# Performance work log

Hardware: AMD Instinct MI355X
Metric: run time of the kernel (lower is better)

The kernel has to match this reference:

```python
import jax, jax.numpy as jnp
import numpy as np

B, P, S, CTX = 64, 10, 200, 512
H, NH, DH = 512, 4, 128      # hidden_dim, num_heads, head_dim
ROLE, NUMR = 32, 10
OUT = 2
T = 100                      # max_steps
LSTM_IN = OUT + 2 + ROLE + CTX  # 548


def setup_inputs() -> dict:
    key = jax.random.key(0)
    ks = jax.random.split(key, 32)
    std = 0.02
    f = jnp.float32
    inp = {
        'context_sequence': jax.random.normal(ks[0], (B, P, S, CTX), f),
        'initial_position': jax.random.normal(ks[1], (B, P, OUT), f),
        'ball_landing': jax.random.normal(ks[2], (B, OUT), f),
        'roles': jax.random.randint(ks[3], (B, P), 0, NUMR),
        'max_steps': T,
        # params
        'role_emb': jax.random.normal(ks[4], (NUMR, ROLE), f) * std,
        'Wc': jax.random.normal(ks[5], (H, CTX), f) * std,
        'bc': jnp.zeros((H,), f),
        'Wq': jax.random.normal(ks[6], (H, H), f) * std,
        'bq': jnp.zeros((H,), f),
        'Wk': jax.random.normal(ks[7], (H, H), f) * std,
        'bk': jnp.zeros((H,), f),
        'Wv': jax.random.normal(ks[8], (H, H), f) * std,
        'bv': jnp.zeros((H,), f),
        'Wo': jax.random.normal(ks[9], (H, H), f) * std,
        'bo': jnp.zeros((H,), f),
        'W_ih0': jax.random.normal(ks[10], (4 * H, LSTM_IN), f) * std,
        'W_hh0': jax.random.normal(ks[11], (4 * H, H), f) * std,
        'b_ih0': jnp.zeros((4 * H,), f),
        'b_hh0': jnp.zeros((4 * H,), f),
        'W_ih1': jax.random.normal(ks[12], (4 * H, H), f) * std,
        'W_hh1': jax.random.normal(ks[13], (4 * H, H), f) * std,
        'b_ih1': jnp.zeros((4 * H,), f),
        'b_hh1': jnp.zeros((4 * H,), f),
        'Wf1': jax.random.normal(ks[14], (H // 2, H), f) * std,
        'bf1': jnp.zeros((H // 2,), f),
        'Wf2': jax.random.normal(ks[15], (OUT, H // 2), f) * std,
        'bf2': jnp.zeros((OUT,), f),
    }
    return inp


def _lstm_cell(x, h, c, Wih, Whh, bih, bhh):
    # torch gate order: i, f, g, o
    g = x @ Wih.T + bih + h @ Whh.T + bhh
    i, fg, gg, o = jnp.split(g, 4, axis=-1)
    cn = jax.nn.sigmoid(fg) * c + jax.nn.sigmoid(i) * jnp.tanh(gg)
    hn = jax.nn.sigmoid(o) * jnp.tanh(cn)
    return hn, cn


def reference(context_sequence, initial_position, ball_landing, roles, max_steps,
              role_emb, Wc, bc, Wq, bq, Wk, bk, Wv, bv, Wo, bo,
              W_ih0, W_hh0, b_ih0, b_hh0, W_ih1, W_hh1, b_ih1, b_hh1,
              Wf1, bf1, Wf2, bf2):
    b, p, s, ctx = context_sequence.shape
    n = b * p
    dt = context_sequence.dtype
    scale = 1.0 / np.sqrt(DH)

    # project context once; hoist K,V (keys/values are constant across steps)
    ctx_proj = context_sequence.reshape(n, s, ctx) @ Wc.T + bc          # [N,S,H]
    K = (ctx_proj @ Wk.T + bk).reshape(n, s, NH, DH)                    # [N,S,h,d]
    V = (ctx_proj @ Wv.T + bv).reshape(n, s, NH, DH)

    role_e = role_emb[roles.reshape(-1)]                                # [N,ROLE]
    ball = jnp.broadcast_to(ball_landing[:, None, :], (b, p, OUT)).reshape(n, OUT)
    pos0 = initial_position.reshape(n, OUT)
    h0 = jnp.zeros((2, n, H), dt)
    c0 = jnp.zeros((2, n, H), dt)

    def step(carry, _):
        h, c, pos = carry
        # query: current pos zero-padded to context_dim, then context_proj
        qin = jnp.concatenate([pos, jnp.zeros((n, ctx - OUT), dt)], axis=-1)
        qp = qin @ Wc.T + bc                                            # [N,H]
        q = (qp @ Wq.T + bq).reshape(n, NH, DH)
        scores = jnp.einsum('nhd,nshd->nhs', q, K) * scale
        w = jax.nn.softmax(scores, axis=-1)
        att = jnp.einsum('nhs,nshd->nhd', w, V).reshape(n, H)
        att = att @ Wo.T + bo                                           # [N,H]
        x = jnp.concatenate([pos, ball, role_e, att], axis=-1)          # [N,548]
        h0n, c0n = _lstm_cell(x, h[0], c[0], W_ih0, W_hh0, b_ih0, b_hh0)
        h1n, c1n = _lstm_cell(h0n, h[1], c[1], W_ih1, W_hh1, b_ih1, b_hh1)
        hid = jax.nn.relu(h1n @ Wf1.T + bf1)
        nxt = hid @ Wf2.T + bf2                                         # [N,2]
        return (jnp.stack([h0n, h1n]), jnp.stack([c0n, c1n]), nxt), nxt

    _, preds = jax.lax.scan(step, (h0, c0, pos0), None, length=max_steps)
    # [T,N,2] -> [B,P,T,2]
    return preds.transpose(1, 0, 2).reshape(b, p, max_steps, OUT)
```

## Files before the change

### kernel.cpp

```cpp
#include <hip/hip_runtime.h>
#include <hip/hip_bf16.h>
#include <cstddef>


typedef _Float16 hx8 __attribute__((ext_vector_type(8)));
typedef float fx4 __attribute__((ext_vector_type(4)));
typedef unsigned long long u64;

#define NSEQ 640
#define TSTEPS 100
#define XC0 1088
#define XC1 1024
#define NBLK 640
#define FL 32

__device__ __forceinline__ float sigm(float x){ return 1.0f/(1.0f+__expf(-x)); }
__device__ __forceinline__ float tanh_(float x){
  x = fminf(fmaxf(x, -15.0f), 15.0f);
  float e = __expf(2.0f*x);
  return (e-1.0f)/(e+1.0f);
}
__device__ __forceinline__ float sel4(float a0,float a1,float a2,float a3,int h){
  float r = a0; r = (h==1)?a1:r; r = (h==2)?a2:r; r = (h==3)?a3:r; return r;
}

__device__ __forceinline__ hx8 ldA(const _Float16* p){
  u64 q0 = __hip_atomic_load((u64*)p,     __ATOMIC_RELAXED, __HIP_MEMORY_SCOPE_AGENT);
  u64 q1 = __hip_atomic_load((u64*)p + 1, __ATOMIC_RELAXED, __HIP_MEMORY_SCOPE_AGENT);
  union { u64 q[2]; hx8 v; } u; u.q[0]=q0; u.q[1]=q1;
  return u.v;
}


__global__ void kF1(const float* __restrict__ Wq, const float* __restrict__ Wc,
                    const float* __restrict__ bc, const float* __restrict__ bq,
                    float* __restrict__ u){
  int r = blockIdx.x*256 + threadIdx.x; if (r >= 512) return;
  float s0=0.f, s1=0.f, s2=0.f;
  for (int k=0;k<512;k++){
    float wq = Wq[r*512+k];
    s0 += wq*Wc[k*512+0];
    s1 += wq*Wc[k*512+1];
    s2 += wq*bc[k];
  }
  u[r]=s0; u[512+r]=s1; u[1024+r]=s2+bq[r];
}

__global__ __launch_bounds__(512) void kF2a(const float* __restrict__ Wk,
                                            const float* __restrict__ u,
                                            float* __restrict__ z){
  int ih = blockIdx.x; int kk = threadIdx.x;
  int i = ih>>2, h = ih&3;
  float s = 0.f;
  for (int d=0; d<128; d++)
    s += Wk[(h*128+d)*512 + kk] * u[i*512 + h*128 + d];
  z[ih*512+kk] = s;
}

__global__ __launch_bounds__(512) void kF2b(const float* __restrict__ z,
                                            const float* __restrict__ Wc,
                                            const float* __restrict__ bc,
                                            const float* __restrict__ bk,
                                            const float* __restrict__ u,
                                            float* __restrict__ Y, float* __restrict__ cc){
  const float scale = 0.08838834764831845f;
  int ih = blockIdx.x; int j = threadIdx.x;
  int i = ih>>2, h = ih&3;
  float s = 0.f;
  for (int kk=0;kk<512;kk++) s += z[ih*512+kk]*Wc[kk*512+j];
  Y[ih*512+j] = s*scale;
  if (j==0){
    float t=0.f;
    for (int kk=0;kk<512;kk++) t += z[ih*512+kk]*bc[kk];
    for (int d=0;d<128;d++) t += u[i*512+h*128+d]*bk[h*128+d];
    cc[ih] = t*scale;
  }
}

__global__ void kFbv(const float* __restrict__ Wv, const float* __restrict__ bc,
                     const float* __restrict__ bv, float* __restrict__ bv2){
  int r = blockIdx.x*256 + threadIdx.x; if (r >= 512) return;
  float s = bv[r];
  for (int k=0;k<512;k++) s += Wv[r*512+k]*bc[k];
  bv2[r]=s;
}

__global__ __launch_bounds__(256) void kgemm(const float* __restrict__ A, int lda, int aoff,
                                             const float* __restrict__ B, int ldb,
                                             float* __restrict__ C, int ldc, int K){
  __shared__ float As[64][16];
  __shared__ float Bs[16][64];
  int tid = threadIdx.x; int tx = tid&15, ty = tid>>4;
  int bx = blockIdx.x, by = blockIdx.y;
  float acc[4][4];
#pragma unroll
  for (int i=0;i<4;i++)
#pragma unroll
    for (int j=0;j<4;j++) acc[i][j]=0.f;
  for (int kk=0; kk<K; kk+=16){
#pragma unroll
    for (int e=0;e<4;e++){
      int id = tid*4+e;
      int r = id>>4, c = id&15;
      As[r][c] = A[(size_t)(by*64+r)*lda + aoff + kk + c];
      int r2 = id>>6, c2 = id&63;
      Bs[r2][c2] = B[(size_t)(kk+r2)*ldb + bx*64 + c2];
    }
    __syncthreads();
#pragma unroll
    for (int k=0;k<16;k++){
      float bvv[4];
#pragma unroll
      for (int j=0;j<4;j++) bvv[j] = Bs[k][tx*4+j];
#pragma unroll
      for (int i=0;i<4;i++){
        float av = As[ty*4+i][k];
#pragma unroll
        for (int j=0;j<4;j++) acc[i][j] += av*bvv[j];
      }
    }
    __syncthreads();
  }
#pragma unroll
  for (int i=0;i<4;i++)
#pragma unroll
    for (int j=0;j<4;j++)
      C[(size_t)(by*64+ty*4+i)*ldc + bx*64+tx*4+j] = acc[i][j];
}

__global__ void ktransp(const float* __restrict__ A, float* __restrict__ AT){
  int idx = blockIdx.x*256 + threadIdx.x;
  int r = idx>>9, c = idx&511;
  AT[c*512 + r] = A[idx];
}

__global__ void kbcat0(const float* __restrict__ Wih0, const float* __restrict__ Wmix,
                       const float* __restrict__ Whh0, _Float16* __restrict__ B){
  int r = blockIdx.x;
  for (int c = threadIdx.x; c < 1088; c += 256){
    float v;
    if (c < 36) v = Wih0[r*548 + c];
    else if (c < 548) v = Wmix[r*512 + (c-36)];
    else if (c < 576) v = 0.f;
    else v = Whh0[r*512 + (c-576)];
    B[(size_t)r*1088 + c] = (_Float16)v;
  }
}

__global__ void kbcat1(const float* __restrict__ Wih1, const float* __restrict__ Whh1,
                       _Float16* __restrict__ B){
  int r = blockIdx.x;
  for (int c = threadIdx.x; c < 1024; c += 256){
    float v = (c < 512) ? Wih1[r*512 + c] : Whh1[r*512 + (c-512)];
    B[(size_t)r*1024 + c] = (_Float16)v;
  }
}

__global__ void kcast(const float* __restrict__ s, _Float16* __restrict__ d, int n){
  int i = blockIdx.x*256 + threadIdx.x;
  if (i < n) d[i] = (_Float16)s[i];
}

__global__ void kbias(const float* __restrict__ Wih0, const float* __restrict__ bo,
                      const float* __restrict__ bih0, const float* __restrict__ bhh0,
                      const float* __restrict__ bih1, const float* __restrict__ bhh1,
                      float* __restrict__ b0, float* __restrict__ b1){
  int j = blockIdx.x*256 + threadIdx.x; if (j >= 2048) return;
  float s = bih0[j]+bhh0[j];
  for (int k=0;k<512;k++) s += Wih0[j*548+36+k]*bo[k];
  b0[j]=s; b1[j]=bih1[j]+bhh1[j];
}


__global__ __launch_bounds__(256) void kP1(const float* __restrict__ ctx,
                                           const float* __restrict__ Y,
                                           const float* __restrict__ cc,
                                           float* __restrict__ W6){
  __shared__ float Yl[6144];
  __shared__ float ccl[12];
  int tid = threadIdx.x; int n = blockIdx.x;
  for (int e = tid; e < 6144; e += 256) Yl[e] = Y[e];
  if (tid < 12) ccl[tid] = cc[tid];
  __syncthreads();
  int wave = tid >> 6, lane = tid & 63;
  for (int it = 0; it < 50; ++it){
    int s = it*4 + wave;
    const float* cp = ctx + ((size_t)n*200 + s)*512;
    float p[12];
#pragma unroll
    for (int i=0;i<12;i++) p[i]=0.f;
    for (int c8 = 0; c8 < 8; ++c8){
      int col = c8*64 + lane;
      float v = cp[col];
#pragma unroll
      for (int i=0;i<12;i++) p[i] += v * Yl[i*512+col];
    }
#pragma unroll
    for (int m = 32; m; m >>= 1){
#pragma unroll
      for (int i=0;i<12;i++) p[i] += __shfl_xor(p[i], m, 64);
    }
    if (lane < 4){
      int h = lane;
      float a  = sel4(p[0],p[1],p[2], p[3], h) + ccl[h];
      float b  = sel4(p[4],p[5],p[6], p[7], h) + ccl[4+h];
      float cp_= sel4(p[8],p[9],p[10],p[11],h) + ccl[8+h];
      float beta = __expf(cp_);
      size_t base = (size_t)(n*24 + h*6)*200 + s;
      W6[base + 0*200] = beta;
      W6[base + 1*200] = beta*a;
      W6[base + 2*200] = beta*b;
      W6[base + 3*200] = beta*a*a*0.5f;
      W6[base + 4*200] = beta*a*b;
      W6[base + 5*200] = beta*b*b*0.5f;
    }
  }
}

__global__ __launch_bounds__(256) void kP2(const float* __restrict__ ctx,
                                           const float* __restrict__ W6,
                                           float* __restrict__ F, float* __restrict__ S){
  __shared__ float w6[4800];
  int tid = threadIdx.x, n = blockIdx.x;
  for (int e = tid; e < 4800; e += 256) w6[e] = W6[(size_t)n*4800 + e];
  __syncthreads();
  float a0[24], a1[24];
#pragma unroll
  for (int r=0;r<24;r++){ a0[r]=0.f; a1[r]=0.f; }
  const float* cp = ctx + (size_t)n*200*512;
  for (int s=0;s<200;s++){
    float v0 = cp[s*512 + tid];
    float v1 = cp[s*512 + tid + 256];
#pragma unroll
    for (int r=0;r<24;r++){ float w = w6[r*200+s]; a0[r]+=w*v0; a1[r]+=w*v1; }
  }
#pragma unroll
  for (int r=0;r<24;r++){
    F[(size_t)(n*24+r)*512 + tid]       = a0[r];
    F[(size_t)(n*24+r)*512 + tid + 256] = a1[r];
  }
  if (tid < 24){
    float s=0.f;
    for (int ss=0; ss<200; ss++) s += w6[tid*200+ss];
    S[n*24+tid]=s;
  }
}

__global__ __launch_bounds__(128) void kP3(const float* __restrict__ F,
                                           const float* __restrict__ WcvT,
                                           float* __restrict__ M){
  __shared__ float Fl[3072];
  int tid = threadIdx.x; int b = blockIdx.x; int n = b>>2, h = b&3;
  for (int e = tid; e < 3072; e += 128) Fl[e] = F[(size_t)(n*24 + h*6)*512 + e];
  __syncthreads();
  float acc[6];
#pragma unroll
  for (int i=0;i<6;i++) acc[i]=0.f;
  for (int k=0;k<512;k++){
    float w = WcvT[k*512 + h*128 + tid];
#pragma unroll
    for (int i=0;i<6;i++) acc[i] += w * Fl[i*512+k];
  }
#pragma unroll
  for (int i=0;i<6;i++) M[(size_t)(n*24+h*6+i)*128 + tid] = acc[i];
}


__global__ __launch_bounds__(512) void kinit(const float* __restrict__ ball,
                    const int* __restrict__ roles, const float* __restrict__ remb,
                    _Float16* __restrict__ x0, _Float16* __restrict__ x1,
                    _Float16* __restrict__ hc0, _Float16* __restrict__ hc1,
                    float* __restrict__ c0, float* __restrict__ c1,
                    unsigned* __restrict__ bar){
  int n = blockIdx.x, tid = threadIdx.x;
  int b = n/10;
  int role = roles[n];
  for (int c = tid; c < XC0; c += 512){
    float v = 0.f;
    if (c>=2 && c<4)       v = ball[b*2 + (c-2)];
    else if (c>=4 && c<36) v = remb[role*32 + (c-4)];
    _Float16 hv = (_Float16)v;
    x0[(size_t)n*XC0+c] = hv;
    x1[(size_t)n*XC0+c] = hv;
  }
  for (int c = tid; c < XC1; c += 512){
    hc0[(size_t)n*XC1+c] = (_Float16)0.f;
    hc1[(size_t)n*XC1+c] = (_Float16)0.f;
  }
  for (int e = tid; e < 512; e += 512){
    c0[n*512+e]=0.f; c1[n*512+e]=0.f;
  }
  if (tid < FL) bar[n*FL + tid] = 0u;
}

__global__ __launch_bounds__(128) void katt0(const float* __restrict__ ipos,
                                             const float* __restrict__ M,
                                             const float* __restrict__ S,
                                             const float* __restrict__ bv2,
                                             _Float16* __restrict__ x){
  int n = blockIdx.x, tid = threadIdx.x;
  float p0 = ipos[n*2], p1 = ipos[n*2+1];
  if (tid==0){ x[(size_t)n*XC0]=(_Float16)p0; x[(size_t)n*XC0+1]=(_Float16)p1; }
  float fa=p0*p0, fb=p0*p1, fc=p1*p1;
  for (int hd = tid; hd < 512; hd += 128){
    int h = hd>>7;
    int sb = n*24 + h*6;
    float den = S[sb] + p0*S[sb+1] + p1*S[sb+2] + fa*S[sb+3] + fb*S[sb+4] + fc*S[sb+5];
    const float* mp = M + (size_t)sb*128 + (hd&127);
    float num = mp[0] + p0*mp[128] + p1*mp[256] + fa*mp[384] + fb*mp[512] + fc*mp[640];
    x[(size_t)n*XC0 + 36 + hd] = (_Float16)(num/den + bv2[hd]);
  }
}


template<int NC>
__device__ __forceinline__ void gates_body(
    const _Float16* __restrict__ A, int lda,
    const _Float16* __restrict__ B,
    const float* __restrict__ bias, float* __restrict__ cst,
    _Float16* __restrict__ h1p, int ldh1, int co1,
    _Float16* __restrict__ h2p, int ldh2, int co2,
    int bx, _Float16* sbase, float (*eps)[32][16]){
  int tid = threadIdx.x, w = tid>>6, lane = tid&63;
  int lr = lane&15, lq = lane>>4;
  int mblk = bx>>5, jb = bx&31;
  int m0 = mblk*32, j0 = jb*16;
  int li = lane>>3, lc = lane&7;
  const _Float16* gA  = A + (size_t)(m0 + w*8 + li)*lda + lc*8;
  const _Float16* gB0 = B + (size_t)(w*512 + j0 + li)*lda + lc*8;
  const _Float16* gB1 = B + (size_t)(w*512 + j0 + 8 + li)*lda + lc*8;
  int sA  = (w*8 + li)*64        + ((lc ^ li)<<3);
  int sB0 = 2048 + (w*16 + li)*64 + ((lc ^ li)<<3);
  int sB1 = 2048 + (w*16 + 8 + li)*64 + ((lc ^ li)<<3);
  int ra7 = lr & 7;
  int fA00 = lr*64        + (((lq  ) ^ ra7)<<3);
  int fA01 = lr*64        + (((lq+4) ^ ra7)<<3);
  int fA10 = (16+lr)*64   + (((lq  ) ^ ra7)<<3);
  int fA11 = (16+lr)*64   + (((lq+4) ^ ra7)<<3);
  int fB0  = 2048 + (w*16+lr)*64 + (((lq  ) ^ ra7)<<3);
  int fB1  = 2048 + (w*16+lr)*64 + (((lq+4) ^ ra7)<<3);
  hx8 pA[3], pB0[3], pB1[3];
#pragma unroll
  for (int i=0;i<3;i++){
    int k = i*64;
    pA[i]  = ldA(gA + k);
    pB0[i] = *(const hx8*)(gB0 + k);
    pB1[i] = *(const hx8*)(gB1 + k);
  }
  fx4 ac0={0.f,0.f,0.f,0.f}, ac1={0.f,0.f,0.f,0.f};
#pragma unroll
  for (int c=0; c<NC; ++c){
    const int s = c % 3;
    _Float16* sb = sbase + (c&1)*6144;
    *(hx8*)(sb + sA)  = pA[s];
    *(hx8*)(sb + sB0) = pB0[s];
    *(hx8*)(sb + sB1) = pB1[s];
    __syncthreads();
    if (c+3 < NC){
      int k = (c+3)*64;
      pA[s]  = ldA(gA + k);
      pB0[s] = *(const hx8*)(gB0 + k);
      pB1[s] = *(const hx8*)(gB1 + k);
    }
    hx8 b0 = *(const hx8*)(sb + fB0);
    hx8 a0 = *(const hx8*)(sb + fA00);
    hx8 a1 = *(const hx8*)(sb + fA10);
    ac0 = __builtin_amdgcn_mfma_f32_16x16x32_f16(a0, b0, ac0, 0,0,0);
    ac1 = __builtin_amdgcn_mfma_f32_16x16x32_f16(a1, b0, ac1, 0,0,0);
    hx8 b1  = *(const hx8*)(sb + fB1);
    hx8 a0b = *(const hx8*)(sb + fA01);
    hx8 a1b = *(const hx8*)(sb + fA11);
    ac0 = __builtin_amdgcn_mfma_f32_16x16x32_f16(a0b, b1, ac0, 0,0,0);
    ac1 = __builtin_amdgcn_mfma_f32_16x16x32_f16(a1b, b1, ac1, 0,0,0);
  }
#pragma unroll
  for (int r=0;r<4;r++){
    eps[w][lq*4+r][lr]    = ac0[r];
    eps[w][16+lq*4+r][lr] = ac1[r];
  }
  __syncthreads();
#pragma unroll
  for (int e=0;e<2;e++){
    int idx = e*256 + tid;
    int ml = idx>>4, j = idx&15;
    float gi = eps[0][ml][j] + bias[       j0+j];
    float gf = eps[1][ml][j] + bias[ 512 + j0+j];
    float gg = eps[2][ml][j] + bias[1024 + j0+j];
    float go = eps[3][ml][j] + bias[1536 + j0+j];
    int ci = (m0+ml)*512 + j0 + j;
    float c_ = cst[ci];
    float cn = sigm(gf)*c_ + sigm(gi)*tanh_(gg);
    float hn = sigm(go)*tanh_(cn);
    cst[ci] = cn;
    _Float16 hh = (_Float16)hn;
    h1p[(size_t)(m0+ml)*ldh1 + co1 + j0 + j] = hh;
    if (h2p) h2p[(size_t)(m0+ml)*ldh2 + co2 + j0 + j] = hh;
  }
}

template<int NC>
__global__ __launch_bounds__(256) void kgates(
    const _Float16* A, int lda, const _Float16* B,
    const float* bias, float* cst,
    _Float16* h1p, int ldh1, int co1,
    _Float16* h2p, int ldh2, int co2){
  __shared__ __align__(16) char smem[32768];
  gates_body<NC>(A, lda, B, bias, cst, h1p, ldh1, co1, h2p, ldh2, co2,
                 blockIdx.x, (_Float16*)smem, (float(*)[32][16])(smem + 24576));
}

__device__ __forceinline__ void s3_body(const _Float16* __restrict__ h1, int ldh,
    const _Float16* __restrict__ Wf1, const float* __restrict__ bf1,
    const float* __restrict__ Wf2, const float* __restrict__ bf2,
    const float* __restrict__ M, const float* __restrict__ S,
    const float* __restrict__ bv2, _Float16* __restrict__ xn,
    float* __restrict__ out, int t, int n0,
    float (*hid)[264], float (*posL)[2], float (*denL)[4]){
  int tid = threadIdx.x, w = tid>>6, lane = tid&63;
  int lr = lane&15, lq = lane>>4;
  fx4 acc[4];
#pragma unroll
  for (int c=0;c<4;c++) acc[c] = (fx4){0.f,0.f,0.f,0.f};
  {
    const _Float16* ap = h1 + (size_t)(n0+lr)*ldh + lq*8;
    for (int ks=0; ks<16; ks++){
      hx8 a = ldA(ap + ks*32);
#pragma unroll
      for (int c=0;c<4;c++){
        const _Float16* bp = Wf1 + (size_t)(w*64 + c*16 + lr)*512 + ks*32 + lq*8;
        acc[c] = __builtin_amdgcn_mfma_f32_16x16x32_f16(a, *(const hx8*)bp, acc[c], 0,0,0);
      }
    }
  }
#pragma unroll
  for (int c=0;c<4;c++)
#pragma unroll
    for (int r=0;r<4;r++){
      int col = w*64 + c*16 + lr;
      hid[lq*4+r][col] = fmaxf(acc[c][r] + bf1[col], 0.f);
    }
  __syncthreads();
  {
    int nn = tid>>4, o = (tid>>3)&1, sub = tid&7;
    float s = 0.f;
#pragma unroll
    for (int k2=0;k2<32;k2++) s += hid[nn][k2*8 + sub] * Wf2[o*256 + k2*8 + sub];
    s += __shfl_xor(s, 1, 64);
    s += __shfl_xor(s, 2, 64);
    s += __shfl_xor(s, 4, 64);
    if (sub==0){
      s += bf2[o];
      out[((size_t)(n0+nn)*TSTEPS + t)*2 + o] = s;
      posL[nn][o] = s;
      xn[(size_t)(n0+nn)*XC0 + o] = (_Float16)s;
    }
  }
  __syncthreads();
  if (tid < 64){
    int nn = tid>>2, h = tid&3;
    float p0 = posL[nn][0], p1 = posL[nn][1];
    int sb = (n0+nn)*24 + h*6;
    float den = S[sb] + p0*S[sb+1] + p1*S[sb+2] + p0*p0*S[sb+3] + p0*p1*S[sb+4] + p1*p1*S[sb+5];
    denL[nn][h] = 1.0f/den;
  }
  __syncthreads();
#pragma unroll
  for (int half=0; half<2; half++){
    int hd = half*256 + tid;
    int h = hd>>7, d = hd&127;
    for (int nn=0; nn<16; nn++){
      float p0 = posL[nn][0], p1 = posL[nn][1];
      float fa = p0*p0, fb = p0*p1, fc = p1*p1;
      const float* mp = M + (size_t)((n0+nn)*24 + h*6)*128 + d;
      float num = mp[0] + p0*mp[128] + p1*mp[256] + fa*mp[384] + fb*mp[512] + fc*mp[640];
      xn[(size_t)(n0+nn)*XC0 + 36 + hd] = (_Float16)(num*denL[nn][h] + bv2[hd]);
    }
  }
}

__global__ __launch_bounds__(256) void ks3b(const _Float16* __restrict__ h1, int ldh,
    const _Float16* __restrict__ Wf1, const float* __restrict__ bf1,
    const float* __restrict__ Wf2, const float* __restrict__ bf2,
    const float* __restrict__ M, const float* __restrict__ S,
    const float* __restrict__ bv2, _Float16* __restrict__ xn,
    float* __restrict__ out, int t){
  __shared__ float hid[16][264];
  __shared__ float posL[16][2];
  __shared__ float denL[16][4];
  s3_body(h1, ldh, Wf1, bf1, Wf2, bf2, M, S, bv2, xn, out, t,
          blockIdx.x*16, hid, posL, denL);
}


__device__ __forceinline__ void garrive(unsigned* bar, int bx, unsigned val){
  __syncthreads();
  if (threadIdx.x == 0)
    __hip_atomic_store(bar + (size_t)bx*FL, val, __ATOMIC_RELEASE,
                       __HIP_MEMORY_SCOPE_AGENT);
}
__device__ __forceinline__ void gwait(unsigned* bar, int bx, unsigned val){
  if (threadIdx.x < 64){
    const unsigned* fp = bar + (size_t)((bx & ~31) + (threadIdx.x & 31))*FL;
    for(;;){
      unsigned v = __hip_atomic_load((unsigned*)fp, __ATOMIC_RELAXED,
                                     __HIP_MEMORY_SCOPE_AGENT);
      if (__ballot(v >= val) == ~0ull) break;
      __builtin_amdgcn_s_sleep(2);
    }
  }
  __syncthreads();
}
__device__ __forceinline__ void gbar32(unsigned* bar, int bx, unsigned val){
  garrive(bar, bx, val);
  gwait(bar, bx, val);
}

struct LoopArgs {
  const _Float16* B0; const _Float16* B1;
  const float* b0; const float* b1;
  float* c0; float* c1;
  _Float16* x0; _Float16* x1; _Float16* h0; _Float16* h1;
  const _Float16* Wf1; const float* bf1; const float* Wf2; const float* bf2;
  const float* M; const float* S; const float* bv2;
  float* out; unsigned* bar;
};

__global__ __launch_bounds__(256, 3) void kloop(LoopArgs a){
  __shared__ __align__(16) char smem[32768];
  _Float16* sbase = (_Float16*)smem;
  float (*eps)[32][16] = (float(*)[32][16])(smem + 24576);
  float (*hid)[264] = (float(*)[264])smem;
  float (*posL)[2] = (float(*)[2])(smem + 16896);
  float (*denL)[4] = (float(*)[4])(smem + 17024);
  int bid = blockIdx.x;
  int mblk = bid>>5, jb = bid&31;
  for (int t = 0; t < TSTEPS; ++t){
    unsigned bb = (unsigned)(t*3);
    _Float16* xin = (t&1) ? a.x1 : a.x0;
    _Float16* xnx = (t&1) ? a.x0 : a.x1;
    _Float16* hin = (t&1) ? a.h1 : a.h0;
    _Float16* hnx = (t&1) ? a.h0 : a.h1;
    gates_body<17>(xin, XC0, a.B0, a.b0, a.c0, hin, XC1, 0, xnx, XC0, 576,
                   bid, sbase, eps);
    gbar32(a.bar, bid, bb+1);
    gates_body<16>(hin, XC1, a.B1, a.b1, a.c1, hnx, XC1, 512,
                   (_Float16*)0, 0, 0, bid, sbase, eps);
    if (jb < 2){
      gbar32(a.bar, bid, bb+2);
      s3_body(hnx + 512, XC1, a.Wf1, a.bf1, a.Wf2, a.bf2, a.M, a.S, a.bv2,
              xnx, a.out, t, mblk*32 + jb*16, hid, posL, denL);
    }
    gbar32(a.bar, bid, bb+3);
  }
}


extern "C" void kernel_launch(void* const* d_in, const int* in_sizes, int n_in,
                              void* d_out, int out_size, void* d_ws, size_t ws_size,
                              hipStream_t stream) {
  const float* ctx   = (const float*)d_in[0];
  const float* ipos  = (const float*)d_in[1];
  const float* ball  = (const float*)d_in[2];
  const int*   roles = (const int*)  d_in[3];
  const float* remb  = (const float*)d_in[5];
  const float* Wc    = (const float*)d_in[6];
  const float* bc    = (const float*)d_in[7];
  const float* Wq    = (const float*)d_in[8];
  const float* bq    = (const float*)d_in[9];
  const float* Wk    = (const float*)d_in[10];
  const float* bk    = (const float*)d_in[11];
  const float* Wv    = (const float*)d_in[12];
  const float* bv    = (const float*)d_in[13];
  const float* Wo    = (const float*)d_in[14];
  const float* bo    = (const float*)d_in[15];
  const float* Wih0  = (const float*)d_in[16];
  const float* Whh0  = (const float*)d_in[17];
  const float* bih0  = (const float*)d_in[18];
  const float* bhh0  = (const float*)d_in[19];
  const float* Wih1  = (const float*)d_in[20];
  const float* Whh1  = (const float*)d_in[21];
  const float* bih1  = (const float*)d_in[22];
  const float* bhh1  = (const float*)d_in[23];
  const float* Wf1   = (const float*)d_in[24];
  const float* bf1   = (const float*)d_in[25];
  const float* Wf2   = (const float*)d_in[26];
  const float* bf2   = (const float*)d_in[27];
  float* out = (float*)d_out;

  char* w = (char*)d_ws;
  auto alloc = [&](size_t bytes){ void* p = (void*)w; w += (bytes + 255) & ~(size_t)255; return p; };
  float* fY    = (float*)alloc(12*512*4);
  float* fcc   = (float*)alloc(12*4);
  float* fu    = (float*)alloc(3*512*4);
  float* fz    = (float*)alloc(12*512*4);
  float* fbv2  = (float*)alloc(512*4);
  float* fWcv  = (float*)alloc((size_t)512*512*4);
  float* fWcvT = (float*)alloc((size_t)512*512*4);
  float* fWmix = (float*)alloc((size_t)2048*512*4);
  _Float16* hB0  = (_Float16*)alloc((size_t)2048*XC0*2);
  _Float16* hB1  = (_Float16*)alloc((size_t)2048*XC1*2);
  _Float16* hWf1 = (_Float16*)alloc((size_t)256*512*2);
  float* fb0 = (float*)alloc(2048*4);
  float* fb1 = (float*)alloc(2048*4);
  float* fW6 = (float*)alloc((size_t)NSEQ*24*200*4);
  float* fS  = (float*)alloc((size_t)NSEQ*24*4);
  float* fF  = (float*)alloc((size_t)NSEQ*24*512*4);
  float* fM  = (float*)alloc((size_t)NSEQ*24*128*4);
  _Float16* xc0 = (_Float16*)alloc((size_t)NSEQ*XC0*2);
  _Float16* xc1 = (_Float16*)alloc((size_t)NSEQ*XC0*2);
  _Float16* hc0 = (_Float16*)alloc((size_t)NSEQ*XC1*2);
  _Float16* hc1 = (_Float16*)alloc((size_t)NSEQ*XC1*2);
  float* fc0 = (float*)alloc((size_t)NSEQ*512*4);
  float* fc1 = (float*)alloc((size_t)NSEQ*512*4);
  unsigned* bar = (unsigned*)alloc((size_t)(NBLK+1)*FL*4);

  kF1 <<<2,  256, 0, stream>>>(Wq, Wc, bc, bq, fu);
  kF2a<<<12, 512, 0, stream>>>(Wk, fu, fz);
  kF2b<<<12, 512, 0, stream>>>(fz, Wc, bc, bk, fu, fY, fcc);
  kFbv<<<2,  256, 0, stream>>>(Wv, bc, bv, fbv2);
  kgemm<<<dim3(8,8),  256, 0, stream>>>(Wv,   512, 0,  Wc, 512, fWcv,  512, 512);
  ktransp<<<1024, 256, 0, stream>>>(fWcv, fWcvT);
  kgemm<<<dim3(8,32), 256, 0, stream>>>(Wih0, 548, 36, Wo, 512, fWmix, 512, 512);
  kbcat0<<<2048, 256, 0, stream>>>(Wih0, fWmix, Whh0, hB0);
  kbcat1<<<2048, 256, 0, stream>>>(Wih1, Whh1, hB1);
  kcast<<<512,  256, 0, stream>>>(Wf1, hWf1, 256*512);
  kbias<<<8, 256, 0, stream>>>(Wih0, bo, bih0, bhh0, bih1, bhh1, fb0, fb1);

  kP1<<<NSEQ, 256, 0, stream>>>(ctx, fY, fcc, fW6);
  kP2<<<NSEQ, 256, 0, stream>>>(ctx, fW6, fF, fS);
  kP3<<<NSEQ*4, 128, 0, stream>>>(fF, fWcvT, fM);

  kinit<<<NSEQ, 512, 0, stream>>>(ball, roles, remb, xc0, xc1, hc0, hc1, fc0, fc1, bar);
  katt0<<<NSEQ, 128, 0, stream>>>(ipos, fM, fS, fbv2, xc0);

  int maxb = 0;
  hipError_t qe = hipOccupancyMaxActiveBlocksPerMultiprocessor(
      &maxb, reinterpret_cast<const void*>(kloop), 256, 0);
  if (qe == hipSuccess && maxb >= 3){
    LoopArgs la;
    la.B0 = hB0; la.B1 = hB1; la.b0 = fb0; la.b1 = fb1;
    la.c0 = fc0; la.c1 = fc1;
    la.x0 = xc0; la.x1 = xc1; la.h0 = hc0; la.h1 = hc1;
    la.Wf1 = hWf1; la.bf1 = bf1; la.Wf2 = Wf2; la.bf2 = bf2;
    la.M = fM; la.S = fS; la.bv2 = fbv2; la.out = out; la.bar = bar;
    kloop<<<NBLK, 256, 0, stream>>>(la);
  } else {
    for (int t = 0; t < TSTEPS; ++t){
      _Float16* xin  = (t&1) ? xc1 : xc0;
      _Float16* xnx  = (t&1) ? xc0 : xc1;
      _Float16* hin  = (t&1) ? hc1 : hc0;
      _Float16* hnx  = (t&1) ? hc0 : hc1;
      kgates<17><<<640, 256, 0, stream>>>(xin, XC0, hB0, fb0, fc0,
                                          hin, XC1, 0, xnx, XC0, 576);
      kgates<16><<<640, 256, 0, stream>>>(hin, XC1, hB1, fb1, fc1,
                                          hnx, XC1, 512, (_Float16*)nullptr, 0, 0);
      ks3b<<<40, 256, 0, stream>>>(hnx + 512, XC1, hWf1, bf1, Wf2, bf2,
                                   fM, fS, fbv2, xnx, out, t);
    }
  }
}
```

Before: 5.110 ms.

## Replace global barriers with fine-grained dataflow flags and split layer-0 K loop

The persistent loop's three barriers per step are replaced with per-block release flags: layer-1 waits only on its 32-block group's layer-0 flags, and the s3 step signals its own flags instead of holding a full barrier. The layer-0 GEMM is split so the h0 recurrent chunks (K chunks 9-16) are computed before waiting on the previous step's s3 output, overlapping that work with the wait. Atomic relaxed loads for A tiles are replaced with plain vector loads, and an acquire fence is added after each wait. Correctness now depends on the flag protocol and on cache visibility of plain loads after the acquire.

```diff
diff --git a/kernel.cpp b/kernel.cpp
--- a/kernel.cpp
+++ b/kernel.cpp
@@ -5,7 +5,6 @@
 
 typedef _Float16 hx8 __attribute__((ext_vector_type(8)));
 typedef float fx4 __attribute__((ext_vector_type(4)));
-typedef unsigned long long u64;
 
 #define NSEQ 640
 #define TSTEPS 100
@@ -22,13 +21,6 @@
 }
 __device__ __forceinline__ float sel4(float a0,float a1,float a2,float a3,int h){
   float r = a0; r = (h==1)?a1:r; r = (h==2)?a2:r; r = (h==3)?a3:r; return r;
-}
-
-__device__ __forceinline__ hx8 ldA(const _Float16* p){
-  u64 q0 = __hip_atomic_load((u64*)p,     __ATOMIC_RELAXED, __HIP_MEMORY_SCOPE_AGENT);
-  u64 q1 = __hip_atomic_load((u64*)p + 1, __ATOMIC_RELAXED, __HIP_MEMORY_SCOPE_AGENT);
-  union { u64 q[2]; hx8 v; } u; u.q[0]=q0; u.q[1]=q1;
-  return u.v;
 }
 
 
@@ -287,10 +279,14 @@
     hc0[(size_t)n*XC1+c] = (_Float16)0.f;
     hc1[(size_t)n*XC1+c] = (_Float16)0.f;
   }
-  for (int e = tid; e < 512; e += 512){
-    c0[n*512+e]=0.f; c1[n*512+e]=0.f;
-  }
-  if (tid < FL) bar[n*FL + tid] = 0u;
+  if (tid < 512){
+    c0[n*512+tid]=0.f; c1[n*512+tid]=0.f;
+  }
+  if (tid < FL){
+    bar[(size_t)n*FL + tid] = 0u;
+    bar[(size_t)(640+n)*FL + tid] = 0u;
+    if (n < 40) bar[(size_t)(1280+n)*FL + tid] = 0u;
+  }
 }
 
 __global__ __launch_bounds__(128) void katt0(const float* __restrict__ ipos,
@@ -313,23 +309,20 @@
 }
 
 
-template<int NC>
-__device__ __forceinline__ void gates_body(
+template<int NCH>
+__device__ __forceinline__ void gates_core(
     const _Float16* __restrict__ A, int lda,
-    const _Float16* __restrict__ B,
-    const float* __restrict__ bias, float* __restrict__ cst,
-    _Float16* __restrict__ h1p, int ldh1, int co1,
-    _Float16* __restrict__ h2p, int ldh2, int co2,
-    int bx, _Float16* sbase, float (*eps)[32][16]){
+    const _Float16* __restrict__ B, int ldb,
+    const int (&ord)[NCH], int m0, int j0,
+    _Float16* __restrict__ sbase, fx4& ac0, fx4& ac1)
+{
   int tid = threadIdx.x, w = tid>>6, lane = tid&63;
   int lr = lane&15, lq = lane>>4;
-  int mblk = bx>>5, jb = bx&31;
-  int m0 = mblk*32, j0 = jb*16;
   int li = lane>>3, lc = lane&7;
   const _Float16* gA  = A + (size_t)(m0 + w*8 + li)*lda + lc*8;
-  const _Float16* gB0 = B + (size_t)(w*512 + j0 + li)*lda + lc*8;
-  const _Float16* gB1 = B + (size_t)(w*512 + j0 + 8 + li)*lda + lc*8;
-  int sA  = (w*8 + li)*64        + ((lc ^ li)<<3);
+  const _Float16* gB0 = B + (size_t)(w*512 + j0 + li)*ldb + lc*8;
+  const _Float16* gB1 = B + (size_t)(w*512 + j0 + 8 + li)*ldb + lc*8;
+  int sA  = (w*8 + li)*64         + ((lc ^ li)<<3);
   int sB0 = 2048 + (w*16 + li)*64 + ((lc ^ li)<<3);
   int sB1 = 2048 + (w*16 + 8 + li)*64 + ((lc ^ li)<<3);
   int ra7 = lr & 7;
@@ -342,23 +335,24 @@
   hx8 pA[3], pB0[3], pB1[3];
 #pragma unroll
   for (int i=0;i<3;i++){
-    int k = i*64;
-    pA[i]  = ldA(gA + k);
-    pB0[i] = *(const hx8*)(gB0 + k);
-    pB1[i] = *(const hx8*)(gB1 + k);
-  }
-  fx4 ac0={0.f,0.f,0.f,0.f}, ac1={0.f,0.f,0.f,0.f};
-#pragma unroll
-  for (int c=0; c<NC; ++c){
+    if (i < NCH){
+      int k = ord[i]*64;
+      pA[i]  = *(const hx8*)(gA  + k);
+      pB0[i] = *(const hx8*)(gB0 + k);
+      pB1[i] = *(const hx8*)(gB1 + k);
+    }
+  }
+#pragma unroll
+  for (int c=0; c<NCH; ++c){
     const int s = c % 3;
     _Float16* sb = sbase + (c&1)*6144;
     *(hx8*)(sb + sA)  = pA[s];
     *(hx8*)(sb + sB0) = pB0[s];
     *(hx8*)(sb + sB1) = pB1[s];
     __syncthreads();
-    if (c+3 < NC){
-      int k = (c+3)*64;
-      pA[s]  = ldA(gA + k);
+    if (c+3 < NCH){
+      int k = ord[c+3]*64;
+      pA[s]  = *(const hx8*)(gA  + k);
       pB0[s] = *(const hx8*)(gB0 + k);
       pB1[s] = *(const hx8*)(gB1 + k);
     }
@@ -373,6 +367,16 @@
     ac0 = __builtin_amdgcn_mfma_f32_16x16x32_f16(a0b, b1, ac0, 0,0,0);
     ac1 = __builtin_amdgcn_mfma_f32_16x16x32_f16(a1b, b1, ac1, 0,0,0);
   }
+}
+
+__device__ __forceinline__ void gates_epi(
+    float (*eps)[32][16], fx4& ac0, fx4& ac1, int m0, int j0,
+    const float* __restrict__ bias, float* __restrict__ cst,
+    _Float16* __restrict__ h1p, int ldh1, int co1,
+    _Float16* __restrict__ h2p, int ldh2, int co2)
+{
+  int tid = threadIdx.x, w = tid>>6, lane = tid&63;
+  int lr = lane&15, lq = lane>>4;
 #pragma unroll
   for (int r=0;r<4;r++){
     eps[w][lq*4+r][lr]    = ac0[r];
@@ -398,17 +402,6 @@
   }
 }
 
-template<int NC>
-__global__ __launch_bounds__(256) void kgates(
-    const _Float16* A, int lda, const _Float16* B,
-    const float* bias, float* cst,
-    _Float16* h1p, int ldh1, int co1,
-    _Float16* h2p, int ldh2, int co2){
-  __shared__ __align__(16) char smem[32768];
-  gates_body<NC>(A, lda, B, bias, cst, h1p, ldh1, co1, h2p, ldh2, co2,
-                 blockIdx.x, (_Float16*)smem, (float(*)[32][16])(smem + 24576));
-}
-
 __device__ __forceinline__ void s3_body(const _Float16* __restrict__ h1, int ldh,
     const _Float16* __restrict__ Wf1, const float* __restrict__ bf1,
     const float* __restrict__ Wf2, const float* __restrict__ bf2,
@@ -424,7 +417,7 @@
   {
     const _Float16* ap = h1 + (size_t)(n0+lr)*ldh + lq*8;
     for (int ks=0; ks<16; ks++){
-      hx8 a = ldA(ap + ks*32);
+      hx8 a = *(const hx8*)(ap + ks*32);
 #pragma unroll
       for (int c=0;c<4;c++){
         const _Float16* bp = Wf1 + (size_t)(w*64 + c*16 + lr)*512 + ks*32 + lq*8;
@@ -476,6 +469,31 @@
       xn[(size_t)(n0+nn)*XC0 + 36 + hd] = (_Float16)(num*denL[nn][h] + bv2[hd]);
     }
   }
+}
+
+
+__global__ __launch_bounds__(256) void kgL0(const _Float16* __restrict__ x,
+    const _Float16* __restrict__ B0, const float* __restrict__ b0,
+    float* __restrict__ c0, _Float16* __restrict__ hin, _Float16* __restrict__ xnx){
+  __shared__ __align__(16) char smem[32768];
+  constexpr int ORD17[17] = {0,1,2,3,4,5,6,7,8,9,10,11,12,13,14,15,16};
+  int bid = blockIdx.x, m0 = (bid>>5)*32, j0 = (bid&31)*16;
+  fx4 ac0={0.f,0.f,0.f,0.f}, ac1={0.f,0.f,0.f,0.f};
+  gates_core<17>(x, XC0, B0, XC0, ORD17, m0, j0, (_Float16*)smem, ac0, ac1);
+  gates_epi((float(*)[32][16])(smem+24576), ac0, ac1, m0, j0, b0, c0,
+            hin, XC1, 0, xnx, XC0, 576);
+}
+
+__global__ __launch_bounds__(256) void kgL1(const _Float16* __restrict__ h,
+    const _Float16* __restrict__ B1, const float* __restrict__ b1,
+    float* __restrict__ c1, _Float16* __restrict__ hnx){
+  __shared__ __align__(16) char smem[32768];
+  constexpr int ORD16[16] = {0,1,2,3,4,5,6,7,8,9,10,11,12,13,14,15};
+  int bid = blockIdx.x, m0 = (bid>>5)*32, j0 = (bid&31)*16;
+  fx4 ac0={0.f,0.f,0.f,0.f}, ac1={0.f,0.f,0.f,0.f};
+  gates_core<16>(h, XC1, B1, XC1, ORD16, m0, j0, (_Float16*)smem, ac0, ac1);
+  gates_epi((float(*)[32][16])(smem+24576), ac0, ac1, m0, j0, b1, c1,
+            hnx, XC1, 512, (_Float16*)nullptr, 0, 0);
 }
 
 __global__ __launch_bounds__(256) void ks3b(const _Float16* __restrict__ h1, int ldh,
@@ -492,27 +510,41 @@
 }
 
 
-__device__ __forceinline__ void garrive(unsigned* bar, int bx, unsigned val){
+__device__ __forceinline__ void arrive_rel(unsigned* flag, unsigned val){
   __syncthreads();
   if (threadIdx.x == 0)
-    __hip_atomic_store(bar + (size_t)bx*FL, val, __ATOMIC_RELEASE,
-                       __HIP_MEMORY_SCOPE_AGENT);
-}
-__device__ __forceinline__ void gwait(unsigned* bar, int bx, unsigned val){
+    __hip_atomic_store(flag, val, __ATOMIC_RELEASE, __HIP_MEMORY_SCOPE_AGENT);
+}
+
+__device__ __forceinline__ void acq_fence(const unsigned* p){
+  unsigned d = __hip_atomic_load(p, __ATOMIC_ACQUIRE, __HIP_MEMORY_SCOPE_AGENT);
+  asm volatile("" :: "v"(d));
+}
+
+__device__ __forceinline__ void wait_group(unsigned* base, unsigned val){
   if (threadIdx.x < 64){
-    const unsigned* fp = bar + (size_t)((bx & ~31) + (threadIdx.x & 31))*FL;
+    const unsigned* p = base + (size_t)(threadIdx.x & 31)*FL;
     for(;;){
-      unsigned v = __hip_atomic_load((unsigned*)fp, __ATOMIC_RELAXED,
-                                     __HIP_MEMORY_SCOPE_AGENT);
+      unsigned v = __hip_atomic_load(p, __ATOMIC_RELAXED, __HIP_MEMORY_SCOPE_AGENT);
       if (__ballot(v >= val) == ~0ull) break;
-      __builtin_amdgcn_s_sleep(2);
-    }
-  }
-  __syncthreads();
-}
-__device__ __forceinline__ void gbar32(unsigned* bar, int bx, unsigned val){
-  garrive(bar, bx, val);
-  gwait(bar, bx, val);
+      __builtin_amdgcn_s_sleep(1);
+    }
+    if (threadIdx.x == 0) acq_fence(base);
+  }
+  __syncthreads();
+}
+
+__device__ __forceinline__ void wait_s3(unsigned* s3f, int m, unsigned val){
+  if (threadIdx.x < 64){
+    const unsigned* p = s3f + (size_t)(2*m + (threadIdx.x & 1))*FL;
+    for(;;){
+      unsigned v = __hip_atomic_load(p, __ATOMIC_RELAXED, __HIP_MEMORY_SCOPE_AGENT);
+      if (__ballot(v >= val) == ~0ull) break;
+      __builtin_amdgcn_s_sleep(1);
+    }
+    if (threadIdx.x == 0) acq_fence(p);
+  }
+  __syncthreads();
 }
 
 struct LoopArgs {
@@ -532,25 +564,40 @@
   float (*hid)[264] = (float(*)[264])smem;
   float (*posL)[2] = (float(*)[2])(smem + 16896);
   float (*denL)[4] = (float(*)[4])(smem + 17024);
+  constexpr int ORD_H0[8] = {9,10,11,12,13,14,15,16};
+  constexpr int ORD_X[9]  = {0,1,2,3,4,5,6,7,8};
+  constexpr int ORD16[16] = {0,1,2,3,4,5,6,7,8,9,10,11,12,13,14,15};
   int bid = blockIdx.x;
-  int mblk = bid>>5, jb = bid&31;
+  int m = bid>>5, jb = bid&31;
+  int m0 = m*32, j0 = jb*16;
+  unsigned* L0own = a.bar + (size_t)bid*FL;
+  unsigned* L1own = a.bar + (size_t)(640+bid)*FL;
+  unsigned* gL0   = a.bar + (size_t)(m*32)*FL;
+  unsigned* gL1   = a.bar + (size_t)(640+m*32)*FL;
+  unsigned* s3f   = a.bar + (size_t)1280*FL;
   for (int t = 0; t < TSTEPS; ++t){
-    unsigned bb = (unsigned)(t*3);
     _Float16* xin = (t&1) ? a.x1 : a.x0;
     _Float16* xnx = (t&1) ? a.x0 : a.x1;
     _Float16* hin = (t&1) ? a.h1 : a.h0;
     _Float16* hnx = (t&1) ? a.h0 : a.h1;
-    gates_body<17>(xin, XC0, a.B0, a.b0, a.c0, hin, XC1, 0, xnx, XC0, 576,
-                   bid, sbase, eps);
-    gbar32(a.bar, bid, bb+1);
-    gates_body<16>(hin, XC1, a.B1, a.b1, a.c1, hnx, XC1, 512,
-                   (_Float16*)0, 0, 0, bid, sbase, eps);
+    fx4 ac0={0.f,0.f,0.f,0.f}, ac1={0.f,0.f,0.f,0.f};
+    gates_core<8>(xin, XC0, a.B0, XC0, ORD_H0, m0, j0, sbase, ac0, ac1);
+    wait_s3(s3f, m, (unsigned)t);
+    gates_core<9>(xin, XC0, a.B0, XC0, ORD_X, m0, j0, sbase, ac0, ac1);
+    gates_epi(eps, ac0, ac1, m0, j0, a.b0, a.c0, hin, XC1, 0, xnx, XC0, 576);
+    arrive_rel(L0own, (unsigned)(t+1));
+    wait_group(gL0, (unsigned)(t+1));
+    ac0 = (fx4){0.f,0.f,0.f,0.f}; ac1 = (fx4){0.f,0.f,0.f,0.f};
+    gates_core<16>(hin, XC1, a.B1, XC1, ORD16, m0, j0, sbase, ac0, ac1);
+    gates_epi(eps, ac0, ac1, m0, j0, a.b1, a.c1, hnx, XC1, 512,
+              (_Float16*)nullptr, 0, 0);
+    arrive_rel(L1own, (unsigned)(t+1));
     if (jb < 2){
-      gbar32(a.bar, bid, bb+2);
+      wait_group(gL1, (unsigned)(t+1));
       s3_body(hnx + 512, XC1, a.Wf1, a.bf1, a.Wf2, a.bf2, a.M, a.S, a.bv2,
-              xnx, a.out, t, mblk*32 + jb*16, hid, posL, denL);
-    }
-    gbar32(a.bar, bid, bb+3);
+              xnx, a.out, t, m0 + jb*16, hid, posL, denL);
+      arrive_rel(s3f + (size_t)(2*m+jb)*FL, (unsigned)(t+1));
+    }
   }
 }
 
@@ -612,7 +659,7 @@
   _Float16* hc1 = (_Float16*)alloc((size_t)NSEQ*XC1*2);
   float* fc0 = (float*)alloc((size_t)NSEQ*512*4);
   float* fc1 = (float*)alloc((size_t)NSEQ*512*4);
-  unsigned* bar = (unsigned*)alloc((size_t)(NBLK+1)*FL*4);
+  unsigned* bar = (unsigned*)alloc((size_t)1320*FL*4);
 
   kF1 <<<2,  256, 0, stream>>>(Wq, Wc, bc, bq, fu);
   kF2a<<<12, 512, 0, stream>>>(Wk, fu, fz);
@@ -650,10 +697,8 @@
       _Float16* xnx  = (t&1) ? xc0 : xc1;
       _Float16* hin  = (t&1) ? hc1 : hc0;
       _Float16* hnx  = (t&1) ? hc0 : hc1;
-      kgates<17><<<640, 256, 0, stream>>>(xin, XC0, hB0, fb0, fc0,
-                                          hin, XC1, 0, xnx, XC0, 576);
-      kgates<16><<<640, 256, 0, stream>>>(hin, XC1, hB1, fb1, fc1,
-                                          hnx, XC1, 512, (_Float16*)nullptr, 0, 0);
+      kgL0<<<640, 256, 0, stream>>>(xin, hB0, fb0, fc0, hin, xnx);
+      kgL1<<<640, 256, 0, stream>>>(hin, hB1, fb1, fc1, hnx);
       ks3b<<<40, 256, 0, stream>>>(hnx + 512, XC1, hWf1, bf1, Wf2, bf2,
                                    fM, fS, fbv2, xnx, out, t);
     }
```

Measured after the change: 4.548 ms. 1.12x faster.
